# Optimization experiments

Hardware: AMD Instinct MI355X
Metric: run time of the kernel (lower is better)

The kernel has to match this reference:

```python
import jax, jax.numpy as jnp
import numpy as np

ROWS, COLS, CH = 10, 10, 8
D = ROWS * COLS * CH  # 800 = state_dim
L = 2                 # num_layers
OUT = 3


def setup_inputs() -> dict:
    key = jax.random.key(0)
    ks = jax.random.split(key, 12)
    B, T, ENC = 64, 32, 128

    def rn(k, shape, sc=0.05):
        return jax.random.normal(k, shape, jnp.float32) * sc

    return {
        "x_flat": jax.random.normal(ks[0], (B, T, ROWS * COLS), jnp.float32),
        "encoder_outputs": jax.random.normal(ks[1], (B, ENC, D), jnp.float32),
        "init_h": jnp.zeros((L, B, ROWS, CH, COLS), jnp.float32),
        "init_c": jnp.zeros((L, B, ROWS, CH, COLS), jnp.float32),
        "conv_w0": rn(ks[2], (4 * CH, 1 + CH, 3)),
        "conv_b0": jnp.zeros((4 * CH,), jnp.float32),
        "conv_w1": rn(ks[3], (4 * CH, 2 * CH, 3)),
        "conv_b1": jnp.zeros((4 * CH,), jnp.float32),
        "inter_w0": rn(ks[4], (2 * D, D)),
        "inter_b0": jnp.zeros((D,), jnp.float32),
        "inter_w1": rn(ks[5], (2 * D, D)),
        "inter_b1": jnp.zeros((D,), jnp.float32),
        "self_w0": rn(ks[6], (2 * D, D)),
        "self_b0": jnp.zeros((D,), jnp.float32),
        "self_w1": rn(ks[7], (2 * D, D)),
        "self_b1": jnp.zeros((D,), jnp.float32),
        "head_w1": rn(ks[8], (D, 200)),
        "head_b1": jnp.zeros((200,), jnp.float32),
        "head_w2": rn(ks[9], (200, 50)),
        "head_b2": jnp.zeros((50,), jnp.float32),
        "head_w3": rn(ks[10], (50, OUT)),
        "head_b3": jnp.zeros((OUT,), jnp.float32),
    }


def reference(x_flat, encoder_outputs, init_h, init_c,
              conv_w0, conv_b0, conv_w1, conv_b1,
              inter_w0, inter_b0, inter_w1, inter_b1,
              self_w0, self_b0, self_w1, self_b1,
              head_w1, head_b1, head_w2, head_b2, head_w3, head_b3):
    B, T, _ = x_flat.shape
    # frames: [T, B, ROWS, 1, COLS]
    xs = jnp.transpose(x_flat.reshape(B, T, ROWS, 1, COLS), (1, 0, 2, 3, 4))
    conv_w = [conv_w0, conv_w1]
    conv_b = [conv_b0, conv_b1]
    iw, ib = [inter_w0, inter_w1], [inter_b0, inter_b1]
    sw, sb = [self_w0, self_w1], [self_b0, self_b1]

    def cell(x, h, c, w, b):
        # row-shared ConvLSTM: 1D conv along cols, weights shared across rows
        z = jnp.concatenate([x, h], axis=2)                  # [B,R,Cin+CH,COLS]
        z2 = z.reshape(B * ROWS, z.shape[2], COLS)
        g = jax.lax.conv_general_dilated(z2, w, (1,), "SAME",
                                         dimension_numbers=("NCW", "OIW", "NCW"))
        g = g.reshape(B, ROWS, 4 * CH, COLS) + b[None, None, :, None]
        i, f, gg, o = jnp.split(g, 4, axis=2)
        c2 = jax.nn.sigmoid(f) * c + jax.nn.sigmoid(i) * jnp.tanh(gg)
        return jax.nn.sigmoid(o) * jnp.tanh(c2), c2

    def inter_attn(h, W, bb):
        # dot-product attention of decoder state over encoder outputs
        w = jax.nn.softmax(jnp.einsum("bd,bld->bl", h, encoder_outputs), axis=-1)
        ctx = jnp.einsum("bl,bld->bd", w, encoder_outputs)
        return jnp.tanh(jnp.concatenate([ctx, h], axis=-1) @ W + bb)

    def self_attn(h, pre, ref, s, W, bb):
        # keys = pre-self states of steps < s, values = refined states of steps < s
        sc = jnp.einsum("bd,tbd->bt", h, pre)                # [B,T]
        mask = (jnp.arange(T) < s)[None, :]
        w = jax.nn.softmax(jnp.where(mask, sc, -1e9), axis=-1)
        ctx = jnp.einsum("bt,tbd->bd", w * mask, ref)
        h2 = jnp.tanh(jnp.concatenate([ctx, h], axis=-1) @ W + bb)
        return jnp.where(s > 0, h2, h)                       # step 0: no history

    def head(v):
        v = jax.nn.relu(v @ head_w1 + head_b1)
        v = jax.nn.relu(v @ head_w2 + head_b2)
        return v @ head_w3 + head_b3

    def step(carry, inp):
        h_all, c_all, pre, ref = carry                       # pre/ref: [L,T,B,D]
        x_t, s = inp
        layer_in = x_t
        hs, cs = [], []
        hv = None
        for l in range(L):
            hr, cn = cell(layer_in, h_all[l], c_all[l], conv_w[l], conv_b[l])
            hv = hr.reshape(B, D)
            hv = inter_attn(hv, iw[l], ib[l])
            pre = pre.at[l, s].set(hv)
            hv = self_attn(hv, pre[l], ref[l], s, sw[l], sb[l])
            ref = ref.at[l, s].set(hv)
            layer_in = hv.reshape(B, ROWS, CH, COLS)
            hs.append(hr)
            cs.append(cn)
        logits = head(hv)
        return (jnp.stack(hs), jnp.stack(cs), pre, ref), logits

    init = (init_h, init_c,
            jnp.zeros((L, T, B, D), x_flat.dtype),
            jnp.zeros((L, T, B, D), x_flat.dtype))
    _, logits = jax.lax.scan(step, init, (xs, jnp.arange(T)))
    return jnp.transpose(logits, (1, 0, 2))                  # [B,T,OUT]
```

## Files before the change

### kernel.cpp

```cpp
#include <hip/hip_runtime.h>
#include <hip/hip_fp16.h>
#include <math.h>

#define BB 64
#define TT 32
#define ENCL 128
#define DD 800
#define TPB 1024
#define NBLK 256

typedef _Float16 h2 __attribute__((ext_vector_type(2)));

__device__ __forceinline__ h2 u2h(unsigned u) { union { unsigned u; h2 h; } c; c.u = u; return c.h; }
__device__ __forceinline__ unsigned pack2(float a, float b) {
    union { unsigned u; h2 h; } c; c.h[0] = (_Float16)a; c.h[1] = (_Float16)b; return c.u;
}
__device__ __forceinline__ float sigf(float x) { return 1.f / (1.f + __expf(-x)); }
__device__ __forceinline__ float wred(float v) {
#pragma unroll
    for (int o = 32; o > 0; o >>= 1) v += __shfl_xor(v, o);
    return v;
}
__device__ __forceinline__ float wmax(float v) {
#pragma unroll
    for (int o = 32; o > 0; o >>= 1) v = fmaxf(v, __shfl_xor(v, o));
    return v;
}

#if __has_builtin(__builtin_amdgcn_fdot2)
__device__ __forceinline__ float FDOT2(h2 a, h2 b, float c) { return __builtin_amdgcn_fdot2(a, b, c, false); }
#else
__device__ __forceinline__ float FDOT2(h2 a, h2 b, float c) {
    return c + (float)a[0] * (float)b[0] + (float)a[1] * (float)b[1];
}
#endif

__device__ __forceinline__ float dot8(uint4 w, uint4 x, float acc) {
    acc = FDOT2(u2h(w.x), u2h(x.x), acc);
    acc = FDOT2(u2h(w.y), u2h(x.y), acc);
    acc = FDOT2(u2h(w.z), u2h(x.z), acc);
    acc = FDOT2(u2h(w.w), u2h(x.w), acc);
    return acc;
}

__device__ __forceinline__ void gsync(unsigned* cnt, int b, unsigned target) {
    __syncthreads();
    if (threadIdx.x == 0) {
        __builtin_amdgcn_fence(__ATOMIC_RELEASE, "agent");
        __hip_atomic_fetch_add(&cnt[b * 32], 1u, __ATOMIC_RELAXED, __HIP_MEMORY_SCOPE_AGENT);
        int guard = 0;
        while (__hip_atomic_load(&cnt[b * 32], __ATOMIC_RELAXED, __HIP_MEMORY_SCOPE_AGENT) < target) {
            __builtin_amdgcn_s_sleep(1);
            if (++guard > (1 << 20)) break;
        }
        __builtin_amdgcn_fence(__ATOMIC_ACQUIRE, "agent");
    }
    __syncthreads();
}

__global__ __launch_bounds__(256) void pack_w1s(const float* __restrict__ W, uint4* __restrict__ out) {
    int i = blockIdx.x * 256 + threadIdx.x;
    if (i >= 160000) return;
    int cs = i % 200;
    int kq = (i / 200) % 200;
    int m  = i / 40000;
    const float* src = W + (size_t)(8 * kq) * 800 + 200 * m + cs;
    uint4 r;
    r.x = pack2(src[0],        src[800]);
    r.y = pack2(src[2 * 800],  src[3 * 800]);
    r.z = pack2(src[4 * 800],  src[5 * 800]);
    r.w = pack2(src[6 * 800],  src[7 * 800]);
    out[i] = r;
}

__global__ __launch_bounds__(256) void pack_w2s(const float* __restrict__ W, uint4* __restrict__ out) {
    int i = blockIdx.x * 256 + threadIdx.x;
    if (i >= 160000) return;
    int c  = i % 800;
    int kq = (i / 800) % 50;
    int m  = i / 40000;
    int kbase = (kq < 25) ? (200 * m + 8 * kq) : (800 + 200 * m + 8 * (kq - 25));
    const float* src = W + (size_t)kbase * 800 + c;
    uint4 r;
    r.x = pack2(src[0],        src[800]);
    r.y = pack2(src[2 * 800],  src[3 * 800]);
    r.z = pack2(src[4 * 800],  src[5 * 800]);
    r.w = pack2(src[6 * 800],  src[7 * 800]);
    out[i] = r;
}

__global__ __launch_bounds__(256) void pack_pairs(const float* __restrict__ in, unsigned* __restrict__ out, int n2) {
    int i = blockIdx.x * 256 + threadIdx.x;
    if (i < n2) out[i] = pack2(in[2 * i], in[2 * i + 1]);
}

__global__ __launch_bounds__(256) void pack_w1(const float* __restrict__ w1, unsigned* __restrict__ out) {
    int i = blockIdx.x * 256 + threadIdx.x;
    if (i >= 400 * 200) return;
    int c = i % 200, kp = i / 200;
    out[i] = pack2(w1[(2 * kp) * 200 + c], w1[(2 * kp + 1) * 200 + c]);
}

__global__ __launch_bounds__(TPB, 1) void decoder_kernel(
    const float* __restrict__ x, const __half* __restrict__ ench,
    const uint4* __restrict__ iw1s0, const uint4* __restrict__ iw1s1,
    const uint4* __restrict__ sw2s0, const uint4* __restrict__ sw2s1,
    const float* __restrict__ ib0, const float* __restrict__ ib1,
    const float* __restrict__ sb0, const float* __restrict__ sb1,
    const float* __restrict__ cw0, const float* __restrict__ cb0,
    const float* __restrict__ cw1, const float* __restrict__ cb1,
    const float* __restrict__ init_h, const float* __restrict__ init_c,
    __half* __restrict__ PREh, __half* __restrict__ REFh,
    float* __restrict__ PP, float* __restrict__ psc, unsigned* __restrict__ cnt,
    const unsigned* __restrict__ w1p, const float* __restrict__ hb1,
    const float* __restrict__ hw2, const float* __restrict__ hb2,
    const float* __restrict__ hw3, const float* __restrict__ hb3,
    float* __restrict__ out)
{
    __shared__ float cwS[2][1536];
    __shared__ float cbS[2][32];
    __shared__ float HC[2][2][DD];
    __shared__ float cin[DD];
    __shared__ float hn[DD];
    __shared__ float ctxf[DD];
    __shared__ float hv_s[200];
    __shared__ alignas(16) unsigned xh[DD];
    __shared__ alignas(16) unsigned xg2[200];
    __shared__ float sc[128];
    __shared__ float pw[128];
    __shared__ float pc1[4][200];

    const int bid = blockIdx.x;
    const int b = bid & 63;
    const int m = bid >> 6;
    const int tid = threadIdx.x;
    const int lane = tid & 63;
    const int wv = tid >> 6;
    const int d2 = tid & 511;
    const int gg = tid >> 9;
    const int c200 = (tid < 800) ? (tid % 200) : 0;
    const int q200 = (tid < 800) ? (tid / 200) : 0;

    const uint4* iwS[2] = {iw1s0, iw1s1};
    const uint4* swS[2] = {sw2s0, sw2s1};
    const float* ib[2] = {ib0, ib1};
    const float* sb[2] = {sb0, sb1};
    const float* cwA[2] = {cw0, cw1};
    const float* cbA[2] = {cb0, cb1};

    for (int l2 = 0; l2 < 2; ++l2) {
        const int cin_l = l2 ? 16 : 9;
        const int nw = 32 * cin_l * 3;
        for (int i = tid; i < nw; i += TPB) {
            int p = i % 3, rest = i / 3;
            int gt = rest & 3, rest2 = rest >> 2;
            int ic = rest2 % cin_l, ch = rest2 / cin_l;
            cwS[l2][(ch * cin_l + ic) * 12 + gt * 3 + p] = cwA[l2][((gt * 8 + ch) * cin_l + ic) * 3 + p];
        }
        for (int i = tid; i < 32; i += TPB) cbS[l2][i] = cbA[l2][i];
        for (int i = tid; i < DD; i += TPB) {
            HC[l2][0][i] = init_h[((size_t)l2 * BB + b) * DD + i];
            HC[l2][1][i] = init_c[((size_t)l2 * BB + b) * DD + i];
        }
    }
    __syncthreads();

    const unsigned* encb = (const unsigned*)ench + (size_t)b * ENCL * 400;
    const uint4* xh4 = (const uint4*)xh;
    float2* pcc = reinterpret_cast<float2*>(&pc1[0][0]);
    unsigned ep = 0;

    for (int s = 0; s < TT; ++s) {
        for (int l = 0; l < 2; ++l) {
            const int cinx = (l == 0) ? 1 : 8;
            const int cin_l = cinx + 8;
            float* PPc = PP + (size_t)((s * 2 + l) & 1) * (NBLK * 800);
            if (l == 0) {
                if (tid < 100) cin[tid] = x[((size_t)b * TT + s) * 100 + tid];
            }
            __syncthreads();
            if (tid < DD) {
                const int col = tid % 10, rch = tid / 10;
                const int ch = rch & 7, r = rch >> 3;
                float g0 = cbS[l][ch], g1 = cbS[l][8 + ch], g2 = cbS[l][16 + ch], g3 = cbS[l][24 + ch];
                for (int ic = 0; ic < cin_l; ++ic) {
                    const float* zb = (ic < cinx)
                        ? ((l == 0) ? &cin[r * 10] : &cin[r * 80 + ic * 10])
                        : &HC[l][0][r * 80 + (ic - cinx) * 10];
                    float z0 = (col > 0) ? zb[col - 1] : 0.f;
                    float z1 = zb[col];
                    float z2 = (col < 9) ? zb[col + 1] : 0.f;
                    const float* wr = &cwS[l][(ch * cin_l + ic) * 12];
                    g0 += z0 * wr[0] + z1 * wr[1] + z2 * wr[2];
                    g1 += z0 * wr[3] + z1 * wr[4] + z2 * wr[5];
                    g2 += z0 * wr[6] + z1 * wr[7] + z2 * wr[8];
                    g3 += z0 * wr[9] + z1 * wr[10] + z2 * wr[11];
                }
                float c2 = sigf(g1) * HC[l][1][tid] + sigf(g0) * tanhf(g2);
                float hnv = sigf(g3) * tanhf(c2);
                hn[tid] = hnv;
                HC[l][1][tid] = c2;
            }
            __syncthreads();
            if (tid < DD) HC[l][0][tid] = hn[tid];
            if (tid < 400) xh[400 + tid] = pack2(hn[2 * tid], hn[2 * tid + 1]);
            __syncthreads();
            {
                const uint4* xq0 = (const uint4*)(xh + 400);
#pragma unroll
                for (int r8 = 0; r8 < 8; ++r8) {
                    const int le = wv * 8 + r8;
                    const uint4* erow4 = (const uint4*)(encb + (size_t)le * 400);
                    float sum = dot8(erow4[lane], xq0[lane], 0.f);
                    if (lane < 36) sum = dot8(erow4[64 + lane], xq0[64 + lane], sum);
                    sum = wred(sum);
                    if (lane == 0) sc[le] = sum;
                }
            }
            __syncthreads();
            if (wv == 0) {
                float v0 = sc[lane], v1 = sc[64 + lane];
                float mm = wmax(fmaxf(v0, v1));
                float e0 = __expf(v0 - mm), e1 = __expf(v1 - mm);
                float S = wred(e0 + e1);
                float inv = 1.f / S;
                pw[lane] = e0 * inv;
                pw[64 + lane] = e1 * inv;
            }
            __syncthreads();
            if (d2 < 400) {
                float a0 = 0.f, a1 = 0.f;
                const unsigned* ep2 = encb + (size_t)(gg * 64) * 400 + d2;
#pragma unroll 8
                for (int k = 0; k < 64; ++k) {
                    h2 ev = u2h(ep2[(size_t)k * 400]);
                    float w = pw[gg * 64 + k];
                    a0 = fmaf(w, (float)ev[0], a0);
                    a1 = fmaf(w, (float)ev[1], a1);
                }
                if (gg == 1) pcc[d2] = make_float2(a0, a1);
                else { ctxf[2 * d2] = a0; ctxf[2 * d2 + 1] = a1; }
            }
            __syncthreads();
            if (tid < 400) xh[tid] = pack2(ctxf[2 * tid] + pcc[tid].x, ctxf[2 * tid + 1] + pcc[tid].y);
            __syncthreads();
            if (tid < 800) {
                float acc = 0.f;
                const uint4* wp = iwS[l] + (size_t)m * 40000 + (size_t)(50 * q200) * 200 + c200;
                const uint4* xv = xh4 + 50 * q200;
#pragma unroll 10
                for (int i = 0; i < 50; ++i)
                    acc = dot8(wp[(size_t)i * 200], xv[i], acc);
                pc1[q200][c200] = acc;
            }
            __syncthreads();
            if (tid < 200) {
                float v = tanhf(pc1[0][tid] + pc1[1][tid] + pc1[2][tid] + pc1[3][tid] + ib[l][200 * m + tid]);
                hv_s[tid] = v;
                PREh[((size_t)(l * BB + b) * TT + s) * DD + 200 * m + tid] = (__half)v;
            }
            __syncthreads();
            if (tid < 100) xh[400 + tid] = pack2(hv_s[2 * tid], hv_s[2 * tid + 1]);
            __syncthreads();

            if (s == 0) {
                if (tid < 200) PPc[((size_t)(b * 4 + m)) * 800 + 200 * m + tid] = hv_s[tid];
                gsync(cnt, b, 4 * (++ep));
                if (tid < 800) {
                    int mo = tid / 200;
                    float v = PPc[((size_t)(b * 4 + mo)) * 800 + tid];
                    cin[tid] = v;
                    if (mo == m) REFh[((size_t)(l * BB + b) * TT + 0) * DD + tid] = (__half)v;
                }
                __syncthreads();
            } else {
                {
                    const uint4* xq4 = (const uint4*)(xh + 400);
                    for (int tp = wv; tp < s; tp += 16) {
                        const uint4* pr4 = (const uint4*)((const unsigned*)PREh
                            + ((size_t)(l * BB + b) * TT + tp) * 400 + 100 * m);
                        float sum = (lane < 25) ? dot8(pr4[lane], xq4[lane], 0.f) : 0.f;
                        sum = wred(sum);
                        if (lane == 0) psc[((size_t)(b * 4 + m)) * 32 + tp] = sum;
                    }
                }
                gsync(cnt, b, 4 * (++ep));
                if (wv == 0) {
                    float v = -3.0e38f;
                    if (lane < s) {
                        v = psc[((size_t)(b * 4 + 0)) * 32 + lane] + psc[((size_t)(b * 4 + 1)) * 32 + lane]
                          + psc[((size_t)(b * 4 + 2)) * 32 + lane] + psc[((size_t)(b * 4 + 3)) * 32 + lane];
                    }
                    float mm = wmax(v);
                    float e = (lane < s) ? __expf(v - mm) : 0.f;
                    float S = wred(e);
                    if (lane < 32) pw[lane] = e / S;
                }
                __syncthreads();
                if (d2 < 400) {
                    float a0 = 0.f, a1 = 0.f;
                    const unsigned* rr = (const unsigned*)REFh + ((size_t)(l * BB + b) * TT) * 400 + d2;
#pragma unroll 4
                    for (int tp = gg; tp < s; tp += 2) {
                        h2 rv = u2h(rr[(size_t)tp * 400]);
                        float w = pw[tp];
                        a0 = fmaf(w, (float)rv[0], a0);
                        a1 = fmaf(w, (float)rv[1], a1);
                    }
                    if (gg == 1) pcc[d2] = make_float2(a0, a1);
                    else { ctxf[2 * d2] = a0; ctxf[2 * d2 + 1] = a1; }
                }
                __syncthreads();
                if (tid < 400) {
                    ctxf[2 * tid] += pcc[tid].x;
                    ctxf[2 * tid + 1] += pcc[tid].y;
                }
                __syncthreads();
                if (tid < 100) xg2[tid] = pack2(ctxf[200 * m + 2 * tid], ctxf[200 * m + 2 * tid + 1]);
                else if (tid < 200) { int i = tid - 100; xg2[tid] = pack2(hv_s[2 * i], hv_s[2 * i + 1]); }
                __syncthreads();
                if (tid < 800) {
                    float acc = 0.f;
                    const uint4* wp = swS[l] + (size_t)m * 40000 + tid;
                    const uint4* xv = (const uint4*)xg2;
#pragma unroll 10
                    for (int kq = 0; kq < 50; ++kq)
                        acc = dot8(wp[(size_t)kq * 800], xv[kq], acc);
                    PPc[((size_t)(b * 4 + m)) * 800 + tid] = acc;
                }
                gsync(cnt, b, 4 * (++ep));
                if (tid < 800) {
                    float o = PPc[((size_t)(b * 4 + 0)) * 800 + tid] + PPc[((size_t)(b * 4 + 1)) * 800 + tid]
                            + PPc[((size_t)(b * 4 + 2)) * 800 + tid] + PPc[((size_t)(b * 4 + 3)) * 800 + tid]
                            + sb[l][tid];
                    float v = tanhf(o);
                    cin[tid] = v;
                    if ((unsigned)(tid - 200 * m) < 200u)
                        REFh[((size_t)(l * BB + b) * TT + s) * DD + tid] = (__half)v;
                }
                __syncthreads();
            }
        }
    }

    gsync(cnt, b, 4 * (++ep));

    unsigned* r8 = reinterpret_cast<unsigned*>(&HC[0][0][0]);
    float* v1s = &cwS[0][0];
    float* v2s = &cwS[0][0] + 1600;
    const unsigned* refu = (const unsigned*)REFh + (((size_t)BB + b) * TT) * 400;
    {
        for (int i = tid; i < 8 * 400; i += TPB)
            r8[i] = refu[(size_t)(m * 8 + i / 400) * 400 + (i % 400)];
        __syncthreads();
        for (int o = tid; o < 1600; o += TPB) {
            int tr = o / 200, c = o % 200;
            float acc = hb1[c];
            const unsigned* rrow = &r8[tr * 400];
#pragma unroll 8
            for (int kp = 0; kp < 400; ++kp)
                acc = FDOT2(u2h(w1p[kp * 200 + c]), u2h(rrow[kp]), acc);
            v1s[o] = fmaxf(acc, 0.f);
        }
        __syncthreads();
        for (int o = tid; o < 400; o += TPB) {
            int tr = o / 50, c = o % 50;
            float acc = hb2[c];
#pragma unroll 4
            for (int k = 0; k < 200; ++k) acc = fmaf(v1s[tr * 200 + k], hw2[k * 50 + c], acc);
            v2s[o] = fmaxf(acc, 0.f);
        }
        __syncthreads();
        for (int o = tid; o < 24; o += TPB) {
            int tr = o / 3, oo = o % 3;
            float acc = hb3[oo];
            for (int k = 0; k < 50; ++k) acc = fmaf(v2s[tr * 50 + k], hw3[k * 3 + oo], acc);
            out[((size_t)b * TT + m * 8 + tr) * 3 + oo] = acc;
        }
    }
}

extern "C" void kernel_launch(void* const* d_in, const int* in_sizes, int n_in,
                              void* d_out, int out_size, void* d_ws, size_t ws_size,
                              hipStream_t stream)
{
    const float* x_flat = (const float*)d_in[0];
    const float* enc    = (const float*)d_in[1];
    const float* init_h = (const float*)d_in[2];
    const float* init_c = (const float*)d_in[3];
    const float* cw0 = (const float*)d_in[4];
    const float* cb0 = (const float*)d_in[5];
    const float* cw1 = (const float*)d_in[6];
    const float* cb1 = (const float*)d_in[7];
    const float* iw0 = (const float*)d_in[8];
    const float* ib0 = (const float*)d_in[9];
    const float* iw1 = (const float*)d_in[10];
    const float* ib1 = (const float*)d_in[11];
    const float* sw0 = (const float*)d_in[12];
    const float* sb0 = (const float*)d_in[13];
    const float* sw1 = (const float*)d_in[14];
    const float* sb1 = (const float*)d_in[15];
    const float* hw1 = (const float*)d_in[16];
    const float* hb1 = (const float*)d_in[17];
    const float* hw2 = (const float*)d_in[18];
    const float* hb2 = (const float*)d_in[19];
    const float* hw3 = (const float*)d_in[20];
    const float* hb3 = (const float*)d_in[21];
    float* out = (float*)d_out;

    char* p = (char*)d_ws;
    uint4* iw1s0 = (uint4*)p; p += (size_t)160000 * 16;
    uint4* iw1s1 = (uint4*)p; p += (size_t)160000 * 16;
    uint4* sw2s0 = (uint4*)p; p += (size_t)160000 * 16;
    uint4* sw2s1 = (uint4*)p; p += (size_t)160000 * 16;
    __half* ench = (__half*)p; p += (size_t)BB * ENCL * DD * 2;
    unsigned* w1p = (unsigned*)p; p += (size_t)400 * 200 * 4;
    __half* PREh = (__half*)p; p += (size_t)2 * BB * TT * DD * 2;
    __half* REFh = (__half*)p; p += (size_t)2 * BB * TT * DD * 2;
    float* PP    = (float*)p; p += (size_t)2 * NBLK * 800 * 4;
    float* psc   = (float*)p; p += (size_t)NBLK * 32 * 4;
    unsigned* cnt = (unsigned*)p; p += (size_t)BB * 32 * 4;

    (void)hipMemsetAsync(cnt, 0, (size_t)BB * 32 * 4, stream);

    pack_w1s<<<625, 256, 0, stream>>>(iw0, iw1s0);
    pack_w1s<<<625, 256, 0, stream>>>(iw1, iw1s1);
    pack_w2s<<<625, 256, 0, stream>>>(sw0, sw2s0);
    pack_w2s<<<625, 256, 0, stream>>>(sw1, sw2s1);
    pack_pairs<<<12800, 256, 0, stream>>>(enc, (unsigned*)ench, BB * ENCL * DD / 2);
    pack_w1<<<313, 256, 0, stream>>>(hw1, w1p);

    decoder_kernel<<<NBLK, TPB, 0, stream>>>(
        x_flat, ench, iw1s0, iw1s1, sw2s0, sw2s1, ib0, ib1, sb0, sb1,
        cw0, cb0, cw1, cb1, init_h, init_c, PREh, REFh, PP, psc, cnt,
        w1p, hb1, hw2, hb2, hw3, hb3, out);
}
```

Before: 4.368 ms.

## Split each batch row across eight blocks and restructure cross-block attention exchange

Doubles the grid so each batch element is handled by eight cooperating blocks, each owning a 100-column slice of the inter and self attention projections. The self-attention weights now use the same column-sliced packing as the inter weights. The partial-score exchange is replaced by exchanging the full projected vector through global memory, after which every block computes all history scores redundantly. Per step this removes one grid sync in layer 1 but adds more blocks that must synchronise and duplicated score work. It relies on all 512 blocks being co-resident for the spin-wait barrier, and the spin guard is shortened.

```diff
diff --git a/kernel.cpp b/kernel.cpp
--- a/kernel.cpp
+++ b/kernel.cpp
@@ -7,7 +7,9 @@
 #define ENCL 128
 #define DD 800
 #define TPB 1024
-#define NBLK 256
+#define NBLK 512
+#define NM 8
+#define SL 100
 
 typedef _Float16 h2 __attribute__((ext_vector_type(2)));
 
@@ -51,20 +53,20 @@
         int guard = 0;
         while (__hip_atomic_load(&cnt[b * 32], __ATOMIC_RELAXED, __HIP_MEMORY_SCOPE_AGENT) < target) {
             __builtin_amdgcn_s_sleep(1);
-            if (++guard > (1 << 20)) break;
+            if (++guard > (1 << 18)) break;
         }
         __builtin_amdgcn_fence(__ATOMIC_ACQUIRE, "agent");
     }
     __syncthreads();
 }
 
-__global__ __launch_bounds__(256) void pack_w1s(const float* __restrict__ W, uint4* __restrict__ out) {
+__global__ __launch_bounds__(256) void pack_ws(const float* __restrict__ W, uint4* __restrict__ out) {
     int i = blockIdx.x * 256 + threadIdx.x;
     if (i >= 160000) return;
-    int cs = i % 200;
-    int kq = (i / 200) % 200;
-    int m  = i / 40000;
-    const float* src = W + (size_t)(8 * kq) * 800 + 200 * m + cs;
+    int cs = i % SL;
+    int kq = (i / SL) % 200;
+    int m  = i / 20000;
+    const float* src = W + (size_t)(8 * kq) * 800 + SL * m + cs;
     uint4 r;
     r.x = pack2(src[0],        src[800]);
     r.y = pack2(src[2 * 800],  src[3 * 800]);
@@ -73,22 +75,6 @@
     out[i] = r;
 }
 
-__global__ __launch_bounds__(256) void pack_w2s(const float* __restrict__ W, uint4* __restrict__ out) {
-    int i = blockIdx.x * 256 + threadIdx.x;
-    if (i >= 160000) return;
-    int c  = i % 800;
-    int kq = (i / 800) % 50;
-    int m  = i / 40000;
-    int kbase = (kq < 25) ? (200 * m + 8 * kq) : (800 + 200 * m + 8 * (kq - 25));
-    const float* src = W + (size_t)kbase * 800 + c;
-    uint4 r;
-    r.x = pack2(src[0],        src[800]);
-    r.y = pack2(src[2 * 800],  src[3 * 800]);
-    r.z = pack2(src[4 * 800],  src[5 * 800]);
-    r.w = pack2(src[6 * 800],  src[7 * 800]);
-    out[i] = r;
-}
-
 __global__ __launch_bounds__(256) void pack_pairs(const float* __restrict__ in, unsigned* __restrict__ out, int n2) {
     int i = blockIdx.x * 256 + threadIdx.x;
     if (i < n2) out[i] = pack2(in[2 * i], in[2 * i + 1]);
@@ -101,17 +87,17 @@
     out[i] = pack2(w1[(2 * kp) * 200 + c], w1[(2 * kp + 1) * 200 + c]);
 }
 
-__global__ __launch_bounds__(TPB, 1) void decoder_kernel(
+__global__ __launch_bounds__(TPB, 8) void decoder_kernel(
     const float* __restrict__ x, const __half* __restrict__ ench,
-    const uint4* __restrict__ iw1s0, const uint4* __restrict__ iw1s1,
-    const uint4* __restrict__ sw2s0, const uint4* __restrict__ sw2s1,
+    const uint4* __restrict__ iws0, const uint4* __restrict__ iws1,
+    const uint4* __restrict__ sws0, const uint4* __restrict__ sws1,
     const float* __restrict__ ib0, const float* __restrict__ ib1,
     const float* __restrict__ sb0, const float* __restrict__ sb1,
     const float* __restrict__ cw0, const float* __restrict__ cb0,
     const float* __restrict__ cw1, const float* __restrict__ cb1,
     const float* __restrict__ init_h, const float* __restrict__ init_c,
     __half* __restrict__ PREh, __half* __restrict__ REFh,
-    float* __restrict__ PP, float* __restrict__ psc, unsigned* __restrict__ cnt,
+    float* __restrict__ PP, unsigned* __restrict__ cnt,
     const unsigned* __restrict__ w1p, const float* __restrict__ hb1,
     const float* __restrict__ hw2, const float* __restrict__ hb2,
     const float* __restrict__ hw3, const float* __restrict__ hb3,
@@ -123,12 +109,10 @@
     __shared__ float cin[DD];
     __shared__ float hn[DD];
     __shared__ float ctxf[DD];
-    __shared__ float hv_s[200];
     __shared__ alignas(16) unsigned xh[DD];
-    __shared__ alignas(16) unsigned xg2[200];
     __shared__ float sc[128];
     __shared__ float pw[128];
-    __shared__ float pc1[4][200];
+    __shared__ alignas(16) float pc1[NM][SL];
 
     const int bid = blockIdx.x;
     const int b = bid & 63;
@@ -138,11 +122,9 @@
     const int wv = tid >> 6;
     const int d2 = tid & 511;
     const int gg = tid >> 9;
-    const int c200 = (tid < 800) ? (tid % 200) : 0;
-    const int q200 = (tid < 800) ? (tid / 200) : 0;
-
-    const uint4* iwS[2] = {iw1s0, iw1s1};
-    const uint4* swS[2] = {sw2s0, sw2s1};
+
+    const uint4* iwS[2] = {iws0, iws1};
+    const uint4* swS[2] = {sws0, sws1};
     const float* ib[2] = {ib0, ib1};
     const float* sb[2] = {sb0, sb1};
     const float* cwA[2] = {cw0, cw1};
@@ -167,14 +149,20 @@
 
     const unsigned* encb = (const unsigned*)ench + (size_t)b * ENCL * 400;
     const uint4* xh4 = (const uint4*)xh;
+    const uint4* xh4h = (const uint4*)(xh + 400);
     float2* pcc = reinterpret_cast<float2*>(&pc1[0][0]);
     unsigned ep = 0;
+    const int kg = tid / SL;
+    const int cs = tid % SL;
 
     for (int s = 0; s < TT; ++s) {
         for (int l = 0; l < 2; ++l) {
             const int cinx = (l == 0) ? 1 : 8;
             const int cin_l = cinx + 8;
-            float* PPc = PP + (size_t)((s * 2 + l) & 1) * (NBLK * 800);
+            const int par = (s * 2 + l) & 1;
+            float* PPa = PP + (size_t)(par * 2 + 0) * (BB * DD);
+            float* PPb = PP + (size_t)(par * 2 + 1) * (BB * DD);
+
             if (l == 0) {
                 if (tid < 100) cin[tid] = x[((size_t)b * TT + s) * 100 + tid];
             }
@@ -205,17 +193,14 @@
             if (tid < DD) HC[l][0][tid] = hn[tid];
             if (tid < 400) xh[400 + tid] = pack2(hn[2 * tid], hn[2 * tid + 1]);
             __syncthreads();
-            {
-                const uint4* xq0 = (const uint4*)(xh + 400);
 #pragma unroll
-                for (int r8 = 0; r8 < 8; ++r8) {
-                    const int le = wv * 8 + r8;
-                    const uint4* erow4 = (const uint4*)(encb + (size_t)le * 400);
-                    float sum = dot8(erow4[lane], xq0[lane], 0.f);
-                    if (lane < 36) sum = dot8(erow4[64 + lane], xq0[64 + lane], sum);
-                    sum = wred(sum);
-                    if (lane == 0) sc[le] = sum;
-                }
+            for (int r8 = 0; r8 < 8; ++r8) {
+                const int le = wv * 8 + r8;
+                const uint4* erow4 = (const uint4*)(encb + (size_t)le * 400);
+                float sum = dot8(erow4[lane], xh4h[lane], 0.f);
+                if (lane < 36) sum = dot8(erow4[64 + lane], xh4h[64 + lane], sum);
+                sum = wred(sum);
+                if (lane == 0) sc[le] = sum;
             }
             __syncthreads();
             if (wv == 0) {
@@ -245,52 +230,50 @@
             if (tid < 400) xh[tid] = pack2(ctxf[2 * tid] + pcc[tid].x, ctxf[2 * tid + 1] + pcc[tid].y);
             __syncthreads();
             if (tid < 800) {
+                const uint4* wp = iwS[l] + (size_t)m * 20000 + (size_t)(kg * 25) * SL + cs;
+                const uint4* xv = xh4 + kg * 25;
                 float acc = 0.f;
-                const uint4* wp = iwS[l] + (size_t)m * 40000 + (size_t)(50 * q200) * 200 + c200;
-                const uint4* xv = xh4 + 50 * q200;
-#pragma unroll 10
-                for (int i = 0; i < 50; ++i)
-                    acc = dot8(wp[(size_t)i * 200], xv[i], acc);
-                pc1[q200][c200] = acc;
-            }
-            __syncthreads();
-            if (tid < 200) {
-                float v = tanhf(pc1[0][tid] + pc1[1][tid] + pc1[2][tid] + pc1[3][tid] + ib[l][200 * m + tid]);
-                hv_s[tid] = v;
-                PREh[((size_t)(l * BB + b) * TT + s) * DD + 200 * m + tid] = (__half)v;
-            }
-            __syncthreads();
-            if (tid < 100) xh[400 + tid] = pack2(hv_s[2 * tid], hv_s[2 * tid + 1]);
-            __syncthreads();
+#pragma unroll 5
+                for (int i = 0; i < 25; ++i)
+                    acc = dot8(wp[(size_t)i * SL], xv[i], acc);
+                pc1[kg][cs] = acc;
+            }
+            __syncthreads();
+            if (tid < SL) {
+                float v = pc1[0][tid] + pc1[1][tid] + pc1[2][tid] + pc1[3][tid]
+                        + pc1[4][tid] + pc1[5][tid] + pc1[6][tid] + pc1[7][tid]
+                        + ib[l][SL * m + tid];
+                v = tanhf(v);
+                PREh[((size_t)(l * BB + b) * TT + s) * DD + SL * m + tid] = (__half)v;
+                if (s == 0) REFh[((size_t)(l * BB + b) * TT + 0) * DD + SL * m + tid] = (__half)v;
+                PPa[(size_t)b * DD + SL * m + tid] = v;
+            }
 
             if (s == 0) {
-                if (tid < 200) PPc[((size_t)(b * 4 + m)) * 800 + 200 * m + tid] = hv_s[tid];
-                gsync(cnt, b, 4 * (++ep));
-                if (tid < 800) {
-                    int mo = tid / 200;
-                    float v = PPc[((size_t)(b * 4 + mo)) * 800 + tid];
-                    cin[tid] = v;
-                    if (mo == m) REFh[((size_t)(l * BB + b) * TT + 0) * DD + tid] = (__half)v;
-                }
-                __syncthreads();
+                if (l == 0) {
+                    gsync(cnt, b, NM * (++ep));
+                    if (tid < DD) cin[tid] = PPa[(size_t)b * DD + tid];
+                    __syncthreads();
+                }
             } else {
-                {
-                    const uint4* xq4 = (const uint4*)(xh + 400);
-                    for (int tp = wv; tp < s; tp += 16) {
-                        const uint4* pr4 = (const uint4*)((const unsigned*)PREh
-                            + ((size_t)(l * BB + b) * TT + tp) * 400 + 100 * m);
-                        float sum = (lane < 25) ? dot8(pr4[lane], xq4[lane], 0.f) : 0.f;
-                        sum = wred(sum);
-                        if (lane == 0) psc[((size_t)(b * 4 + m)) * 32 + tp] = sum;
-                    }
-                }
-                gsync(cnt, b, 4 * (++ep));
+                gsync(cnt, b, NM * (++ep));
+                if (tid < 400) {
+                    float a = PPa[(size_t)b * DD + 2 * tid];
+                    float bb2 = PPa[(size_t)b * DD + 2 * tid + 1];
+                    xh[400 + tid] = pack2(a, bb2);
+                }
+                __syncthreads();
+                for (int tp = wv; tp < s; tp += 16) {
+                    const uint4* pr4 = (const uint4*)((const unsigned*)PREh
+                        + ((size_t)(l * BB + b) * TT + tp) * 400);
+                    float sum = dot8(pr4[lane], xh4h[lane], 0.f);
+                    if (lane < 36) sum = dot8(pr4[64 + lane], xh4h[64 + lane], sum);
+                    sum = wred(sum);
+                    if (lane == 0) sc[tp] = sum;
+                }
+                __syncthreads();
                 if (wv == 0) {
-                    float v = -3.0e38f;
-                    if (lane < s) {
-                        v = psc[((size_t)(b * 4 + 0)) * 32 + lane] + psc[((size_t)(b * 4 + 1)) * 32 + lane]
-                          + psc[((size_t)(b * 4 + 2)) * 32 + lane] + psc[((size_t)(b * 4 + 3)) * 32 + lane];
-                    }
+                    float v = (lane < s) ? sc[lane] : -3.0e38f;
                     float mm = wmax(v);
                     float e = (lane < s) ? __expf(v - mm) : 0.f;
                     float S = wred(e);
@@ -311,72 +294,67 @@
                     else { ctxf[2 * d2] = a0; ctxf[2 * d2 + 1] = a1; }
                 }
                 __syncthreads();
-                if (tid < 400) {
-                    ctxf[2 * tid] += pcc[tid].x;
-                    ctxf[2 * tid + 1] += pcc[tid].y;
-                }
-                __syncthreads();
-                if (tid < 100) xg2[tid] = pack2(ctxf[200 * m + 2 * tid], ctxf[200 * m + 2 * tid + 1]);
-                else if (tid < 200) { int i = tid - 100; xg2[tid] = pack2(hv_s[2 * i], hv_s[2 * i + 1]); }
+                if (tid < 400) xh[tid] = pack2(ctxf[2 * tid] + pcc[tid].x, ctxf[2 * tid + 1] + pcc[tid].y);
                 __syncthreads();
                 if (tid < 800) {
+                    const uint4* wp = swS[l] + (size_t)m * 20000 + (size_t)(kg * 25) * SL + cs;
+                    const uint4* xv = xh4 + kg * 25;
                     float acc = 0.f;
-                    const uint4* wp = swS[l] + (size_t)m * 40000 + tid;
-                    const uint4* xv = (const uint4*)xg2;
-#pragma unroll 10
-                    for (int kq = 0; kq < 50; ++kq)
-                        acc = dot8(wp[(size_t)kq * 800], xv[kq], acc);
-                    PPc[((size_t)(b * 4 + m)) * 800 + tid] = acc;
-                }
-                gsync(cnt, b, 4 * (++ep));
-                if (tid < 800) {
-                    float o = PPc[((size_t)(b * 4 + 0)) * 800 + tid] + PPc[((size_t)(b * 4 + 1)) * 800 + tid]
-                            + PPc[((size_t)(b * 4 + 2)) * 800 + tid] + PPc[((size_t)(b * 4 + 3)) * 800 + tid]
-                            + sb[l][tid];
-                    float v = tanhf(o);
-                    cin[tid] = v;
-                    if ((unsigned)(tid - 200 * m) < 200u)
-                        REFh[((size_t)(l * BB + b) * TT + s) * DD + tid] = (__half)v;
-                }
-                __syncthreads();
+#pragma unroll 5
+                    for (int i = 0; i < 25; ++i)
+                        acc = dot8(wp[(size_t)i * SL], xv[i], acc);
+                    pc1[kg][cs] = acc;
+                }
+                __syncthreads();
+                if (tid < SL) {
+                    float v = pc1[0][tid] + pc1[1][tid] + pc1[2][tid] + pc1[3][tid]
+                            + pc1[4][tid] + pc1[5][tid] + pc1[6][tid] + pc1[7][tid]
+                            + sb[l][SL * m + tid];
+                    v = tanhf(v);
+                    REFh[((size_t)(l * BB + b) * TT + s) * DD + SL * m + tid] = (__half)v;
+                    if (l == 0) PPb[(size_t)b * DD + SL * m + tid] = v;
+                }
+                if (l == 0) {
+                    gsync(cnt, b, NM * (++ep));
+                    if (tid < DD) cin[tid] = PPb[(size_t)b * DD + tid];
+                    __syncthreads();
+                }
             }
         }
     }
 
-    gsync(cnt, b, 4 * (++ep));
+    gsync(cnt, b, NM * (++ep));
 
     unsigned* r8 = reinterpret_cast<unsigned*>(&HC[0][0][0]);
     float* v1s = &cwS[0][0];
-    float* v2s = &cwS[0][0] + 1600;
+    float* v2s = &cwS[0][0] + 800;
     const unsigned* refu = (const unsigned*)REFh + (((size_t)BB + b) * TT) * 400;
-    {
-        for (int i = tid; i < 8 * 400; i += TPB)
-            r8[i] = refu[(size_t)(m * 8 + i / 400) * 400 + (i % 400)];
-        __syncthreads();
-        for (int o = tid; o < 1600; o += TPB) {
-            int tr = o / 200, c = o % 200;
-            float acc = hb1[c];
-            const unsigned* rrow = &r8[tr * 400];
+    for (int i = tid; i < 4 * 400; i += TPB)
+        r8[i] = refu[(size_t)(m * 4 + i / 400) * 400 + (i % 400)];
+    __syncthreads();
+    for (int o = tid; o < 800; o += TPB) {
+        int tr = o / 200, c = o % 200;
+        float acc = hb1[c];
+        const unsigned* rrow = &r8[tr * 400];
 #pragma unroll 8
-            for (int kp = 0; kp < 400; ++kp)
-                acc = FDOT2(u2h(w1p[kp * 200 + c]), u2h(rrow[kp]), acc);
-            v1s[o] = fmaxf(acc, 0.f);
-        }
-        __syncthreads();
-        for (int o = tid; o < 400; o += TPB) {
-            int tr = o / 50, c = o % 50;
-            float acc = hb2[c];
+        for (int kp = 0; kp < 400; ++kp)
+            acc = FDOT2(u2h(w1p[kp * 200 + c]), u2h(rrow[kp]), acc);
+        v1s[o] = fmaxf(acc, 0.f);
+    }
+    __syncthreads();
+    for (int o = tid; o < 200; o += TPB) {
+        int tr = o / 50, c = o % 50;
+        float acc = hb2[c];
 #pragma unroll 4
-            for (int k = 0; k < 200; ++k) acc = fmaf(v1s[tr * 200 + k], hw2[k * 50 + c], acc);
-            v2s[o] = fmaxf(acc, 0.f);
-        }
-        __syncthreads();
-        for (int o = tid; o < 24; o += TPB) {
-            int tr = o / 3, oo = o % 3;
-            float acc = hb3[oo];
-            for (int k = 0; k < 50; ++k) acc = fmaf(v2s[tr * 50 + k], hw3[k * 3 + oo], acc);
-            out[((size_t)b * TT + m * 8 + tr) * 3 + oo] = acc;
-        }
+        for (int k = 0; k < 200; ++k) acc = fmaf(v1s[tr * 200 + k], hw2[k * 50 + c], acc);
+        v2s[o] = fmaxf(acc, 0.f);
+    }
+    __syncthreads();
+    for (int o = tid; o < 12; o += TPB) {
+        int tr = o / 3, oo = o % 3;
+        float acc = hb3[oo];
+        for (int k = 0; k < 50; ++k) acc = fmaf(v2s[tr * 50 + k], hw3[k * 3 + oo], acc);
+        out[((size_t)b * TT + m * 4 + tr) * 3 + oo] = acc;
     }
 }
 
@@ -409,29 +387,28 @@
     float* out = (float*)d_out;
 
     char* p = (char*)d_ws;
-    uint4* iw1s0 = (uint4*)p; p += (size_t)160000 * 16;
-    uint4* iw1s1 = (uint4*)p; p += (size_t)160000 * 16;
-    uint4* sw2s0 = (uint4*)p; p += (size_t)160000 * 16;
-    uint4* sw2s1 = (uint4*)p; p += (size_t)160000 * 16;
+    uint4* iws0 = (uint4*)p; p += (size_t)160000 * 16;
+    uint4* iws1 = (uint4*)p; p += (size_t)160000 * 16;
+    uint4* sws0 = (uint4*)p; p += (size_t)160000 * 16;
+    uint4* sws1 = (uint4*)p; p += (size_t)160000 * 16;
     __half* ench = (__half*)p; p += (size_t)BB * ENCL * DD * 2;
     unsigned* w1p = (unsigned*)p; p += (size_t)400 * 200 * 4;
     __half* PREh = (__half*)p; p += (size_t)2 * BB * TT * DD * 2;
     __half* REFh = (__half*)p; p += (size_t)2 * BB * TT * DD * 2;
-    float* PP    = (float*)p; p += (size_t)2 * NBLK * 800 * 4;
-    float* psc   = (float*)p; p += (size_t)NBLK * 32 * 4;
+    float* PP    = (float*)p; p += (size_t)4 * BB * DD * 4;
     unsigned* cnt = (unsigned*)p; p += (size_t)BB * 32 * 4;
 
     (void)hipMemsetAsync(cnt, 0, (size_t)BB * 32 * 4, stream);
 
-    pack_w1s<<<625, 256, 0, stream>>>(iw0, iw1s0);
-    pack_w1s<<<625, 256, 0, stream>>>(iw1, iw1s1);
-    pack_w2s<<<625, 256, 0, stream>>>(sw0, sw2s0);
-    pack_w2s<<<625, 256, 0, stream>>>(sw1, sw2s1);
+    pack_ws<<<625, 256, 0, stream>>>(iw0, iws0);
+    pack_ws<<<625, 256, 0, stream>>>(iw1, iws1);
+    pack_ws<<<625, 256, 0, stream>>>(sw0, sws0);
+    pack_ws<<<625, 256, 0, stream>>>(sw1, sws1);
     pack_pairs<<<12800, 256, 0, stream>>>(enc, (unsigned*)ench, BB * ENCL * DD / 2);
     pack_w1<<<313, 256, 0, stream>>>(hw1, w1p);
 
     decoder_kernel<<<NBLK, TPB, 0, stream>>>(
-        x_flat, ench, iw1s0, iw1s1, sw2s0, sw2s1, ib0, ib1, sb0, sb1,
-        cw0, cb0, cw1, cb1, init_h, init_c, PREh, REFh, PP, psc, cnt,
+        x_flat, ench, iws0, iws1, sws0, sws1, ib0, ib1, sb0, sb1,
+        cw0, cb0, cw1, cb1, init_h, init_c, PREh, REFh, PP, cnt,
         w1p, hb1, hw2, hb2, hw3, hb3, out);
 }
```

Result: slower. 5.258 ms (+20.4%).
